# Kernel optimization log

Measured on AMD Instinct MI355X. Metric: run time of the kernel, lower is better.

The kernel has to match this reference:

```python
import jax, jax.numpy as jnp
import numpy as np

HEAD_DIM = 128
Q_HEADS = 24
KV_HEADS = 8
TARGET_KV_HEADS = 32
HIDDEN = 3072


def setup_inputs() -> dict:
    key = jax.random.key(0)
    ks = jax.random.split(key, 8)
    bsz, q_len = 4, 2048
    return {
        "hidden_states": jax.random.normal(ks[0], (bsz, q_len, HIDDEN), jnp.float32),
        "rope_rotary_cos_sin": jax.random.normal(ks[1], (bsz, q_len, HEAD_DIM), jnp.float32),
        "context_lengths": jax.random.randint(ks[2], (bsz,), 0, q_len, jnp.int32),
        "kvcache_start_index": jax.random.randint(ks[3], (bsz,), 0, q_len, jnp.int32),
        "kv_cache": jax.random.normal(ks[4], (bsz, 2, KV_HEADS, 4096, HEAD_DIM), jnp.float32),
        "Wq": jax.random.normal(ks[5], (Q_HEADS * HEAD_DIM, HIDDEN), jnp.float32) * 0.02,
        "Wk": jax.random.normal(ks[6], (KV_HEADS * HEAD_DIM, HIDDEN), jnp.float32) * 0.02,
        "Wv": jax.random.normal(ks[7], (KV_HEADS * HEAD_DIM, HIDDEN), jnp.float32) * 0.02,
        "Wo": jax.random.normal(jax.random.fold_in(key, 99), (HIDDEN, Q_HEADS * HEAD_DIM), jnp.float32) * 0.02,
    }


def reference(hidden_states, rope_rotary_cos_sin, context_lengths, kvcache_start_index,
              kv_cache, Wq, Wk, Wv, Wo):
    bsz, q_len, _ = hidden_states.shape
    # QKV projections (nn.Linear, no bias): y = x @ W^T
    q = jnp.einsum('bsh,dh->bsd', hidden_states, Wq)
    k = jnp.einsum('bsh,dh->bsd', hidden_states, Wk)
    v = jnp.einsum('bsh,dh->bsd', hidden_states, Wv)
    # [b, heads, s, d]
    q = q.reshape(bsz, q_len, Q_HEADS, HEAD_DIM).transpose(0, 2, 1, 3)
    k = k.reshape(bsz, q_len, KV_HEADS, HEAD_DIM).transpose(0, 2, 1, 3)
    v = v.reshape(bsz, q_len, KV_HEADS, HEAD_DIM).transpose(0, 2, 1, 3)
    # GQA head padding: each kv head repeated `repeats` times contiguously
    repeats = TARGET_KV_HEADS // KV_HEADS
    k = jnp.repeat(k, repeats, axis=1)
    v = jnp.repeat(v, repeats, axis=1)
    qk_scale = jnp.asarray(HEAD_DIM ** -0.5, dtype=hidden_states.dtype)
    q = q * qk_scale
    # trt::fake_attention is a placeholder: returns (query.clone(), kv_cache.clone()).
    # Faithful to the source math: attn_output = scaled query; kv_cache passes through.
    attn_output = q  # [b, Q_HEADS, s, d]
    attn_output = attn_output.transpose(0, 2, 1, 3).reshape(bsz, q_len, Q_HEADS * HEAD_DIM)
    # current (3072) == o_proj.in_features (3072): no repeat/truncate branch taken
    out = jnp.einsum('bsd,od->bso', attn_output, Wo)
    return (out, kv_cache)
```

## Files before the change

kernel.cpp:

```cpp
#include <hip/hip_runtime.h>


typedef __attribute__((ext_vector_type(8))) __bf16 bf16x8;
typedef __attribute__((ext_vector_type(4))) float f32x4;

__device__ __forceinline__ unsigned short f2bf(float f) {
  union { float f; unsigned u; } v; v.f = f;
  unsigned r = v.u + 0x7fffu + ((v.u >> 16) & 1u);
  return (unsigned short)(r >> 16);
}

__global__ void cast_f32_to_bf16(const float4* __restrict__ in,
                                 ushort4* __restrict__ out, int n4) {
  int i = blockIdx.x * blockDim.x + threadIdx.x;
  int stride = gridDim.x * blockDim.x;
  for (; i < n4; i += stride) {
    float4 v = in[i];
    ushort4 o;
    o.x = f2bf(v.x); o.y = f2bf(v.y); o.z = f2bf(v.z); o.w = f2bf(v.w);
    out[i] = o;
  }
}

__global__ void transpose_cast(const float* __restrict__ in,
                               ushort* __restrict__ out, int R, int C) {
  __shared__ float tile[32][33];
  const int tc = blockIdx.x * 32;
  const int tr = blockIdx.y * 32;
  const int lx = threadIdx.x & 31;
  const int ly = threadIdx.x >> 5;
#pragma unroll
  for (int i = 0; i < 32; i += 8)
    tile[ly + i][lx] = in[(size_t)(tr + ly + i) * C + (tc + lx)];
  __syncthreads();
#pragma unroll
  for (int i = 0; i < 32; i += 8)
    out[(size_t)(tc + ly + i) * R + (tr + lx)] = f2bf(tile[lx][ly + i]);
}

typedef const __attribute__((address_space(1))) void* gptr_t;
typedef __attribute__((address_space(3))) void* lptr_t;

__device__ __forceinline__ void gload16(const void* g, void* l) {
  __builtin_amdgcn_global_load_lds((gptr_t)g, (lptr_t)l, 16, 0, 0);
}

#define BAR   do { asm volatile("" ::: "memory"); __builtin_amdgcn_s_barrier(); asm volatile("" ::: "memory"); } while (0)
#define LGKM0 asm volatile("s_waitcnt lgkmcnt(0)" ::: "memory")
#define VM(n) asm volatile("s_waitcnt vmcnt(" #n ")" ::: "memory")

template <int OUT_BF16>
__global__ __launch_bounds__(512, 2)
void gemm_k(const ushort* __restrict__ A, const ushort* __restrict__ B,
            void* __restrict__ Cv, int M, int N, int K, float scale) {
  __shared__ __align__(16) char smem[114688];

  const int t    = threadIdx.x;
  const int w    = t >> 6;
  const int lane = t & 63;
  const int wr   = w >> 2;
  const int wc   = w & 3;
  const int fr   = lane & 15;
  const int g    = lane >> 4;

  const int nwg = gridDim.x;
  const int cpx = nwg >> 3;
  const int wg  = (blockIdx.x & 7) * cpx + (blockIdx.x >> 3);
  const int nbx = N / 192;
  const int bx  = wg % nbx, by = wg / nbx;
  const int rowBase = by * 256, colBase = bx * 192;

  const int sr   = lane >> 3;
  const int scol = ((lane & 7) ^ sr) << 3;
  const ushort* Ag = A + (size_t)(rowBase + w * 8 + sr) * K + scol;
  const ushort* Bg = B + (size_t)(colBase + w * 8 + sr) * K + scol;
  const int wofs = w * 1024;

#define STAGE_A_LOW(kt)  do { char* d_ = smem + ((kt) & 1) * 57344 + wofs;          \
    const ushort* s_ = Ag + (size_t)(kt) * 64;                                      \
    gload16(s_, d_); gload16(s_ + (size_t)64 * K, d_ + 8192); } while (0)
#define STAGE_A_HIGH(kt) do { char* d_ = smem + ((kt) & 1) * 57344 + 16384 + wofs;  \
    const ushort* s_ = Ag + (size_t)128 * K + (size_t)(kt) * 64;                    \
    gload16(s_, d_); gload16(s_ + (size_t)64 * K, d_ + 8192); } while (0)
#define STAGE_B(kt)      do { char* d_ = smem + ((kt) & 1) * 57344 + 32768 + wofs;  \
    const ushort* s_ = Bg + (size_t)(kt) * 64;                                      \
    gload16(s_, d_); gload16(s_ + (size_t)64 * K, d_ + 8192);                       \
    gload16(s_ + (size_t)128 * K, d_ + 16384); } while (0)

  const int aBase = (wr * 128 + fr) * 128;
  const int bBase = 32768 + (wc * 48 + fr) * 128;
  const int cs0   = (g ^ (fr & 7)) << 4;
  const int cs1   = ((4 | g) ^ (fr & 7)) << 4;

#define READ_A8(dst, bo, MH) do {                                     \
    const char* p_ = smem + (bo) + aBase + (MH) * 8192;               \
    dst[0] = *(const bf16x8*)(p_ + cs0);                              \
    dst[1] = *(const bf16x8*)(p_ + 2048 + cs0);                       \
    dst[2] = *(const bf16x8*)(p_ + 4096 + cs0);                       \
    dst[3] = *(const bf16x8*)(p_ + 6144 + cs0);                       \
    dst[4] = *(const bf16x8*)(p_ + cs1);                              \
    dst[5] = *(const bf16x8*)(p_ + 2048 + cs1);                       \
    dst[6] = *(const bf16x8*)(p_ + 4096 + cs1);                       \
    dst[7] = *(const bf16x8*)(p_ + 6144 + cs1); } while (0)
#define READ_B6(dst, bo) do {                                         \
    const char* p_ = smem + (bo) + bBase;                             \
    dst[0] = *(const bf16x8*)(p_ + cs0);                              \
    dst[1] = *(const bf16x8*)(p_ + 2048 + cs0);                       \
    dst[2] = *(const bf16x8*)(p_ + 4096 + cs0);                       \
    dst[3] = *(const bf16x8*)(p_ + cs1);                              \
    dst[4] = *(const bf16x8*)(p_ + 2048 + cs1);                       \
    dst[5] = *(const bf16x8*)(p_ + 4096 + cs1); } while (0)
#define MFMA24(MH, A8, B6) do {                                       \
    _Pragma("unroll") for (int mi_ = 0; mi_ < 4; ++mi_)               \
    _Pragma("unroll") for (int ni_ = 0; ni_ < 3; ++ni_)               \
      acc[(MH) * 4 + mi_][ni_] = __builtin_amdgcn_mfma_f32_16x16x32_bf16( \
          A8[mi_], B6[ni_], acc[(MH) * 4 + mi_][ni_], 0, 0, 0);       \
    _Pragma("unroll") for (int mi_ = 0; mi_ < 4; ++mi_)               \
    _Pragma("unroll") for (int ni_ = 0; ni_ < 3; ++ni_)               \
      acc[(MH) * 4 + mi_][ni_] = __builtin_amdgcn_mfma_f32_16x16x32_bf16( \
          A8[4 + mi_], B6[3 + ni_], acc[(MH) * 4 + mi_][ni_], 0, 0, 0); } while (0)

  f32x4 acc[8][3];
#pragma unroll
  for (int m = 0; m < 8; ++m)
#pragma unroll
    for (int n = 0; n < 3; ++n)
      acc[m][n] = f32x4{0.f, 0.f, 0.f, 0.f};

  bf16x8 aM0[8], aM1[8], BA[6], BB[6];

  const int nt = K >> 6;

  STAGE_A_LOW(0); STAGE_B(0); STAGE_A_HIGH(0);
  STAGE_A_LOW(1); STAGE_B(1); STAGE_A_HIGH(1);
  VM(7);
  BAR;
  READ_A8(aM0, 0, 0);
  READ_B6(BA, 0);
  LGKM0;
  BAR;

#define TILE_BODY(T, BC, BN_) do {                                            \
    const int bo_  = ((T) & 1) * 57344;                                       \
    const int bon_ = 57344 - bo_;                                             \
    const bool stg_ = (T) + 2 < nt;                                           \
                                                                     \
    READ_A8(aM1, bo_, 1);                                                     \
    if (stg_) STAGE_B((T) + 2);                                               \
    BAR; LGKM0;                                                               \
    __builtin_amdgcn_s_setprio(1); MFMA24(0, aM0, BC); __builtin_amdgcn_s_setprio(0); \
    if ((T) < nt - 2) { VM(3); } else { VM(0); }                              \
    BAR;                                                                      \
                                                                     \
    if ((T) + 1 < nt) { READ_A8(aM0, bon_, 0); READ_B6(BN_, bon_); }          \
    if (stg_) { STAGE_A_LOW((T) + 2); STAGE_A_HIGH((T) + 2); }                \
    BAR; LGKM0;                                                               \
    __builtin_amdgcn_s_setprio(1); MFMA24(1, aM1, BC); __builtin_amdgcn_s_setprio(0); \
    BAR;                                                                      \
  } while (0)

  for (int TT = 0; TT < nt; TT += 2) {
    TILE_BODY(TT, BA, BB);
    TILE_BODY(TT + 1, BB, BA);
  }

#undef TILE_BODY
#undef STAGE_A_LOW
#undef STAGE_A_HIGH
#undef STAGE_B
#undef READ_A8
#undef READ_B6
#undef MFMA24

  const int orow = rowBase + wr * 128 + (g << 2);
  const int ocol = colBase + wc * 48 + fr;
#pragma unroll
  for (int mi = 0; mi < 8; ++mi)
#pragma unroll
    for (int ni = 0; ni < 3; ++ni)
#pragma unroll
      for (int i = 0; i < 4; ++i) {
        const size_t idx = (size_t)(orow + mi * 16 + i) * N + (ocol + ni * 16);
        float v = acc[mi][ni][i] * scale;
        if (OUT_BF16) ((ushort*)Cv)[idx] = f2bf(v);
        else          ((float*)Cv)[idx]  = v;
      }
}

extern "C" void kernel_launch(void* const* d_in, const int* in_sizes, int n_in,
                              void* d_out, int out_size, void* d_ws, size_t ws_size,
                              hipStream_t stream) {
  const float* hs = (const float*)d_in[0];
  const float* kv = (const float*)d_in[4];
  const float* Wq = (const float*)d_in[5];
  const float* Wo = (const float*)d_in[8];

  const int M = 8192, H = 3072;
  const int OUT_ELEMS = M * H;

  float* out = (float*)d_out;

  ushort* Xb   = (ushort*)d_ws;
  ushort* Wob  = Xb + (size_t)M * H;
  ushort* WqTb = Wob + (size_t)H * H;
  ushort* Wb   = (ushort*)(out + OUT_ELEMS);

  cast_f32_to_bf16<<<2048, 256, 0, stream>>>((const float4*)hs, (ushort4*)Xb, (M * H) / 4);
  cast_f32_to_bf16<<<1024, 256, 0, stream>>>((const float4*)Wo, (ushort4*)Wob, (H * H) / 4);
  transpose_cast<<<dim3(H / 32, H / 32), 256, 0, stream>>>(Wq, WqTb, H, H);

  const float qk_scale = 0.08838834764831845f;
  gemm_k<1><<<(H / 256) * (H / 192), 512, 0, stream>>>(Wob, WqTb, (void*)Wb, H, H, H, qk_scale);
  gemm_k<0><<<(M / 256) * (H / 192), 512, 0, stream>>>(Xb, Wb, (void*)out, M, H, H, 1.0f);

  hipMemcpyAsync(out + OUT_ELEMS, kv, (size_t)in_sizes[4] * sizeof(float),
                 hipMemcpyDeviceToDevice, stream);
}
```

Before: 351.8 us.

## Switch GEMM to 256x256 tiles with K=32 steps and 4-slot LDS ring

Replaces the 256x192 output tile with a 256x256 tile and shrinks the K step from 64 to 32, using a four-slot LDS ring of 32 KB per slot. The swizzle, staging addresses and fragment reads are redone to match, and each wave now computes 128x64 with 16 MFMAs per half-step. The aim is more arithmetic per loaded byte and a squarer tile that divides 3072 evenly. The costs are more accumulator registers (32 f32x4), twice as many K iterations with barriers per FLOP, and only 144 or 384 workgroups, which may fill the 256 CUs unevenly.

```diff
diff --git a/kernel.cpp b/kernel.cpp
--- a/kernel.cpp
+++ b/kernel.cpp
@@ -51,9 +51,9 @@
 
 template <int OUT_BF16>
 __global__ __launch_bounds__(512, 2)
-void gemm_k(const ushort* __restrict__ A, const ushort* __restrict__ B,
+void gemm_p(const ushort* __restrict__ A, const ushort* __restrict__ B,
             void* __restrict__ Cv, int M, int N, int K, float scale) {
-  __shared__ __align__(16) char smem[114688];
+  __shared__ __align__(16) char smem[131072];
 
   const int t    = threadIdx.x;
   const int w    = t >> 6;
@@ -66,118 +66,102 @@
   const int nwg = gridDim.x;
   const int cpx = nwg >> 3;
   const int wg  = (blockIdx.x & 7) * cpx + (blockIdx.x >> 3);
-  const int nbx = N / 192;
+  const int nbx = N >> 8;
   const int bx  = wg % nbx, by = wg / nbx;
-  const int rowBase = by * 256, colBase = bx * 192;
-
-  const int sr   = lane >> 3;
-  const int scol = ((lane & 7) ^ sr) << 3;
-  const ushort* Ag = A + (size_t)(rowBase + w * 8 + sr) * K + scol;
-  const ushort* Bg = B + (size_t)(colBase + w * 8 + sr) * K + scol;
-  const int wofs = w * 1024;
-
-#define STAGE_A_LOW(kt)  do { char* d_ = smem + ((kt) & 1) * 57344 + wofs;          \
-    const ushort* s_ = Ag + (size_t)(kt) * 64;                                      \
-    gload16(s_, d_); gload16(s_ + (size_t)64 * K, d_ + 8192); } while (0)
-#define STAGE_A_HIGH(kt) do { char* d_ = smem + ((kt) & 1) * 57344 + 16384 + wofs;  \
-    const ushort* s_ = Ag + (size_t)128 * K + (size_t)(kt) * 64;                    \
-    gload16(s_, d_); gload16(s_ + (size_t)64 * K, d_ + 8192); } while (0)
-#define STAGE_B(kt)      do { char* d_ = smem + ((kt) & 1) * 57344 + 32768 + wofs;  \
-    const ushort* s_ = Bg + (size_t)(kt) * 64;                                      \
-    gload16(s_, d_); gload16(s_ + (size_t)64 * K, d_ + 8192);                       \
-    gload16(s_ + (size_t)128 * K, d_ + 16384); } while (0)
-
-  const int aBase = (wr * 128 + fr) * 128;
-  const int bBase = 32768 + (wc * 48 + fr) * 128;
-  const int cs0   = (g ^ (fr & 7)) << 4;
-  const int cs1   = ((4 | g) ^ (fr & 7)) << 4;
-
-#define READ_A8(dst, bo, MH) do {                                     \
-    const char* p_ = smem + (bo) + aBase + (MH) * 8192;               \
-    dst[0] = *(const bf16x8*)(p_ + cs0);                              \
-    dst[1] = *(const bf16x8*)(p_ + 2048 + cs0);                       \
-    dst[2] = *(const bf16x8*)(p_ + 4096 + cs0);                       \
-    dst[3] = *(const bf16x8*)(p_ + 6144 + cs0);                       \
-    dst[4] = *(const bf16x8*)(p_ + cs1);                              \
-    dst[5] = *(const bf16x8*)(p_ + 2048 + cs1);                       \
-    dst[6] = *(const bf16x8*)(p_ + 4096 + cs1);                       \
-    dst[7] = *(const bf16x8*)(p_ + 6144 + cs1); } while (0)
-#define READ_B6(dst, bo) do {                                         \
-    const char* p_ = smem + (bo) + bBase;                             \
-    dst[0] = *(const bf16x8*)(p_ + cs0);                              \
-    dst[1] = *(const bf16x8*)(p_ + 2048 + cs0);                       \
-    dst[2] = *(const bf16x8*)(p_ + 4096 + cs0);                       \
-    dst[3] = *(const bf16x8*)(p_ + cs1);                              \
-    dst[4] = *(const bf16x8*)(p_ + 2048 + cs1);                       \
-    dst[5] = *(const bf16x8*)(p_ + 4096 + cs1); } while (0)
-#define MFMA24(MH, A8, B6) do {                                       \
-    _Pragma("unroll") for (int mi_ = 0; mi_ < 4; ++mi_)               \
-    _Pragma("unroll") for (int ni_ = 0; ni_ < 3; ++ni_)               \
+  const int rowBase = by * 256, colBase = bx * 256;
+
+  const int srow = t >> 2;
+  const int scol = ((t & 3) ^ ((t >> 3) & 3)) << 3;
+  const ushort* Ag = A + (size_t)(rowBase + srow) * K + scol;
+  const ushort* Bg = B + (size_t)(colBase + srow) * K + scol;
+  const int wofs = w << 10;
+
+#define SLOT(T) (((T) & 3) * 32768)
+#define STAGE_A(kt) do { char* d_ = smem + SLOT(kt) + wofs;            \
+    const ushort* s_ = Ag + (size_t)(kt) * 32;                         \
+    gload16(s_, d_); gload16(s_ + (size_t)128 * K, d_ + 8192); } while (0)
+#define STAGE_B(kt) do { char* d_ = smem + SLOT(kt) + 16384 + wofs;    \
+    const ushort* s_ = Bg + (size_t)(kt) * 32;                         \
+    gload16(s_, d_); gload16(s_ + (size_t)128 * K, d_ + 8192); } while (0)
+
+  const int cs   = (g ^ ((fr >> 1) & 3)) << 4;
+  const int aOff = (wr * 128 + fr) * 64 + cs;
+  const int bOff = 16384 + (wc * 64 + fr) * 64 + cs;
+
+#define READ_A(dst, so, MH) do {                                       \
+    const char* p_ = smem + (so) + aOff + (MH) * 4096;                 \
+    dst[0] = *(const bf16x8*)(p_);                                     \
+    dst[1] = *(const bf16x8*)(p_ + 1024);                              \
+    dst[2] = *(const bf16x8*)(p_ + 2048);                              \
+    dst[3] = *(const bf16x8*)(p_ + 3072); } while (0)
+#define READ_B(dst, so) do {                                           \
+    const char* p_ = smem + (so) + bOff;                               \
+    dst[0] = *(const bf16x8*)(p_);                                     \
+    dst[1] = *(const bf16x8*)(p_ + 1024);                              \
+    dst[2] = *(const bf16x8*)(p_ + 2048);                              \
+    dst[3] = *(const bf16x8*)(p_ + 3072); } while (0)
+#define MFMA16(MH, A4, B4) do {                                        \
+    _Pragma("unroll") for (int mi_ = 0; mi_ < 4; ++mi_)                \
+    _Pragma("unroll") for (int ni_ = 0; ni_ < 4; ++ni_)                \
       acc[(MH) * 4 + mi_][ni_] = __builtin_amdgcn_mfma_f32_16x16x32_bf16( \
-          A8[mi_], B6[ni_], acc[(MH) * 4 + mi_][ni_], 0, 0, 0);       \
-    _Pragma("unroll") for (int mi_ = 0; mi_ < 4; ++mi_)               \
-    _Pragma("unroll") for (int ni_ = 0; ni_ < 3; ++ni_)               \
-      acc[(MH) * 4 + mi_][ni_] = __builtin_amdgcn_mfma_f32_16x16x32_bf16( \
-          A8[4 + mi_], B6[3 + ni_], acc[(MH) * 4 + mi_][ni_], 0, 0, 0); } while (0)
-
-  f32x4 acc[8][3];
+          A4[mi_], B4[ni_], acc[(MH) * 4 + mi_][ni_], 0, 0, 0); } while (0)
+
+  f32x4 acc[8][4];
 #pragma unroll
   for (int m = 0; m < 8; ++m)
 #pragma unroll
-    for (int n = 0; n < 3; ++n)
+    for (int n = 0; n < 4; ++n)
       acc[m][n] = f32x4{0.f, 0.f, 0.f, 0.f};
 
-  bf16x8 aM0[8], aM1[8], BA[6], BB[6];
-
-  const int nt = K >> 6;
-
-  STAGE_A_LOW(0); STAGE_B(0); STAGE_A_HIGH(0);
-  STAGE_A_LOW(1); STAGE_B(1); STAGE_A_HIGH(1);
-  VM(7);
+  bf16x8 Af0[4], Af1[4], Bp[4], Bq[4];
+
+  const int nt = K >> 5;
+
+  STAGE_A(0); STAGE_B(0);
+  STAGE_A(1); STAGE_B(1);
+  VM(4);
   BAR;
-  READ_A8(aM0, 0, 0);
-  READ_B6(BA, 0);
-  LGKM0;
-  BAR;
+  READ_A(Af0, SLOT(0), 0);
+  READ_B(Bp, SLOT(0));
 
 #define TILE_BODY(T, BC, BN_) do {                                            \
-    const int bo_  = ((T) & 1) * 57344;                                       \
-    const int bon_ = 57344 - bo_;                                             \
+    const int so_  = SLOT(T);                                                 \
+    const int so1_ = SLOT((T) + 1);                                           \
     const bool stg_ = (T) + 2 < nt;                                           \
                                                                      \
-    READ_A8(aM1, bo_, 1);                                                     \
+    READ_A(Af1, so_, 1);                                                      \
+    if (stg_) STAGE_A((T) + 2);                                               \
+    BAR; LGKM0;                                                               \
+    __builtin_amdgcn_s_setprio(1); MFMA16(0, Af0, BC); __builtin_amdgcn_s_setprio(0); \
+    if ((T) < nt - 2) { VM(2); } else { VM(0); }                              \
+    BAR;                                                                      \
+                                                                     \
+    if ((T) + 1 < nt) { READ_A(Af0, so1_, 0); READ_B(BN_, so1_); }            \
     if (stg_) STAGE_B((T) + 2);                                               \
     BAR; LGKM0;                                                               \
-    __builtin_amdgcn_s_setprio(1); MFMA24(0, aM0, BC); __builtin_amdgcn_s_setprio(0); \
-    if ((T) < nt - 2) { VM(3); } else { VM(0); }                              \
-    BAR;                                                                      \
-                                                                     \
-    if ((T) + 1 < nt) { READ_A8(aM0, bon_, 0); READ_B6(BN_, bon_); }          \
-    if (stg_) { STAGE_A_LOW((T) + 2); STAGE_A_HIGH((T) + 2); }                \
-    BAR; LGKM0;                                                               \
-    __builtin_amdgcn_s_setprio(1); MFMA24(1, aM1, BC); __builtin_amdgcn_s_setprio(0); \
+    __builtin_amdgcn_s_setprio(1); MFMA16(1, Af1, BC); __builtin_amdgcn_s_setprio(0); \
     BAR;                                                                      \
   } while (0)
 
-  for (int TT = 0; TT < nt; TT += 2) {
-    TILE_BODY(TT, BA, BB);
-    TILE_BODY(TT + 1, BB, BA);
+  for (int T = 0; T < nt; T += 2) {
+    TILE_BODY(T, Bp, Bq);
+    TILE_BODY(T + 1, Bq, Bp);
   }
 
 #undef TILE_BODY
-#undef STAGE_A_LOW
-#undef STAGE_A_HIGH
+#undef STAGE_A
 #undef STAGE_B
-#undef READ_A8
-#undef READ_B6
-#undef MFMA24
+#undef READ_A
+#undef READ_B
+#undef MFMA16
+#undef SLOT
 
   const int orow = rowBase + wr * 128 + (g << 2);
-  const int ocol = colBase + wc * 48 + fr;
+  const int ocol = colBase + wc * 64 + fr;
 #pragma unroll
   for (int mi = 0; mi < 8; ++mi)
 #pragma unroll
-    for (int ni = 0; ni < 3; ++ni)
+    for (int ni = 0; ni < 4; ++ni)
 #pragma unroll
       for (int i = 0; i < 4; ++i) {
         const size_t idx = (size_t)(orow + mi * 16 + i) * N + (ocol + ni * 16);
@@ -210,8 +194,8 @@
   transpose_cast<<<dim3(H / 32, H / 32), 256, 0, stream>>>(Wq, WqTb, H, H);
 
   const float qk_scale = 0.08838834764831845f;
-  gemm_k<1><<<(H / 256) * (H / 192), 512, 0, stream>>>(Wob, WqTb, (void*)Wb, H, H, H, qk_scale);
-  gemm_k<0><<<(M / 256) * (H / 192), 512, 0, stream>>>(Xb, Wb, (void*)out, M, H, H, 1.0f);
+  gemm_p<1><<<(H / 256) * (H / 256), 512, 0, stream>>>(Wob, WqTb, (void*)Wb, H, H, H, qk_scale);
+  gemm_p<0><<<(M / 256) * (H / 256), 512, 0, stream>>>(Xb, Wb, (void*)out, M, H, H, 1.0f);
 
   hipMemcpyAsync(out + OUT_ELEMS, kv, (size_t)in_sizes[4] * sizeof(float),
                  hipMemcpyDeviceToDevice, stream);
```

New measurement: 369.1 us. 1.05x slower.
